# Kernel tuning notes

Hardware: AMD Instinct MI355X
Metric: run time of the kernel (lower is better)

## Reference

```python
import jax, jax.numpy as jnp
import numpy as np


def setup_inputs() -> dict:
    key = jax.random.key(0)
    kx, ke = jax.random.split(key)
    B, D, H, W, K = 64, 64, 32, 32, 512
    x = jax.random.normal(kx, (B, D, H, W), dtype=jnp.float32)
    # matches nn.init.normal_(weight, mean=0.0, std=2*D**-0.5)
    emb = jax.random.normal(ke, (D, K), dtype=jnp.float32) * (2.0 * D ** -0.5)
    return {"x": x, "emb": emb}


def reference(x, emb):
    # x: (B, D, *spatial), emb: (D, K)
    B, D = x.shape[0], x.shape[1]
    spatial = x.shape[2:]
    xf = jnp.moveaxis(x, 1, -1).reshape(B, -1, D)  # (B, N, D)
    scores = -2.0 * jnp.einsum('bnd,dk->bnk', xf, emb) + jnp.sum(emb * emb, axis=0)  # (B, N, K)
    argmin = jnp.argmin(scores, axis=-1)  # (B, N) int
    quant = jnp.take(emb.T, argmin, axis=0)  # (B, N, D) gather from codebook
    result = jnp.moveaxis(quant.reshape(B, *spatial, D), -1, 1)  # (B, D, *spatial)
    return result, argmin.reshape(B, *spatial)
```

## Files before the change

### kernel.cpp

```cpp
#include <hip/hip_runtime.h>


constexpr int D    = 64;
constexpr int K    = 512;
constexpr int HW   = 1024;
constexpr int ROWS = 64;
constexpr int CK   = 128;
constexpr int NCH  = K / CK;

__global__ __launch_bounds__(256, 3) void vq_kernel(
    const float* __restrict__ x,
    const float* __restrict__ emb,
    float* __restrict__ out_q,
    float* __restrict__ out_idx)
{
    __shared__ float xs[D][ROWS];
    __shared__ float es[D][CK];
    __shared__ float e2s[K];
    __shared__ int   kfin[ROWS];

    const int tid = threadIdx.x;
    const int ct  = tid & 15;
    const int rg  = tid >> 4;
    const int r0  = blockIdx.x * ROWS;
    const int b   = r0 >> 10;
    const int n0  = r0 & (HW - 1);

    const float* xg = x + ((size_t)b * D) * HW + n0;

    #pragma unroll
    for (int h = 0; h < 2; ++h) {
        const int k = h * 256 + tid;
        float s = 0.f;
        #pragma unroll
        for (int d = 0; d < D; ++d) {
            const float v = emb[d * K + k];
            s = fmaf(v, v, s);
        }
        e2s[k] = s;
    }

    #pragma unroll
    for (int p = 0; p < 4; ++p) {
        const int li = p * 256 + tid;
        const int d  = li >> 4;
        const int r4 = (li & 15) << 2;
        const float4 v = *reinterpret_cast<const float4*>(xg + (size_t)d * HW + r4);
        *reinterpret_cast<float4*>(&xs[d][r4]) = v;
    }

    float best[4] = {3.4e38f, 3.4e38f, 3.4e38f, 3.4e38f};
    int   bidx[4] = {0, 0, 0, 0};

    for (int ch = 0; ch < NCH; ++ch) {
        __syncthreads();

        #pragma unroll
        for (int p = 0; p < 8; ++p) {
            const int li = p * 256 + tid;
            const int d  = li >> 5;
            const int c4 = (li & 31) << 2;
            const float4 v = *reinterpret_cast<const float4*>(emb + d * K + ch * CK + c4);
            *reinterpret_cast<float4*>(&es[d][c4]) = v;
        }
        __syncthreads();

        float acc[4][8];
        #pragma unroll
        for (int j = 0; j < 4; ++j)
            #pragma unroll
            for (int i = 0; i < 8; ++i) acc[j][i] = 0.f;

        #pragma unroll
        for (int d = 0; d < D; ++d) {
            const float4 xv  = *reinterpret_cast<const float4*>(&xs[d][rg << 2]);
            const float4 ev0 = *reinterpret_cast<const float4*>(&es[d][ct << 3]);
            const float4 ev1 = *reinterpret_cast<const float4*>(&es[d][(ct << 3) + 4]);
            const float* xf  = reinterpret_cast<const float*>(&xv);
            const float* ef0 = reinterpret_cast<const float*>(&ev0);
            const float* ef1 = reinterpret_cast<const float*>(&ev1);
            #pragma unroll
            for (int j = 0; j < 4; ++j) {
                const float xj = xf[j];
                #pragma unroll
                for (int i = 0; i < 4; ++i) {
                    acc[j][i]     = fmaf(xj, ef0[i], acc[j][i]);
                    acc[j][i + 4] = fmaf(xj, ef1[i], acc[j][i + 4]);
                }
            }
        }

        const int kb = ch * CK + (ct << 3);
        const float4 q0 = *reinterpret_cast<const float4*>(&e2s[kb]);
        const float4 q1 = *reinterpret_cast<const float4*>(&e2s[kb + 4]);
        const float* qf0 = reinterpret_cast<const float*>(&q0);
        const float* qf1 = reinterpret_cast<const float*>(&q1);
        #pragma unroll
        for (int j = 0; j < 4; ++j) {
            #pragma unroll
            for (int i = 0; i < 8; ++i) {
                const float e2 = (i < 4) ? qf0[i] : qf1[i - 4];
                const float s  = fmaf(-2.f, acc[j][i], e2);
                if (s < best[j]) { best[j] = s; bidx[j] = kb + i; }
            }
        }
    }

    #pragma unroll
    for (int m = 1; m < 16; m <<= 1) {
        #pragma unroll
        for (int j = 0; j < 4; ++j) {
            const float ob = __shfl_xor(best[j], m, 64);
            const int   oi = __shfl_xor(bidx[j], m, 64);
            if (ob < best[j] || (ob == best[j] && oi < bidx[j])) {
                best[j] = ob; bidx[j] = oi;
            }
        }
    }

    if (ct == 0) {
        #pragma unroll
        for (int j = 0; j < 4; ++j) {
            kfin[(rg << 2) + j] = bidx[j];
            __builtin_nontemporal_store((float)bidx[j], &out_idx[r0 + (rg << 2) + j]);
        }
    }
    __syncthreads();

    const int row = tid & 63;
    const int dg  = tid >> 6;
    const int kq  = kfin[row];
    float* oq = out_q + ((size_t)b * D) * HW + n0 + row;
    #pragma unroll
    for (int j = 0; j < 16; ++j) {
        const int d = (dg << 4) + j;
        __builtin_nontemporal_store(emb[d * K + kq], &oq[(size_t)d * HW]);
    }
}

extern "C" void kernel_launch(void* const* d_in, const int* in_sizes, int n_in,
                              void* d_out, int out_size, void* d_ws, size_t ws_size,
                              hipStream_t stream)
{
    const float* x   = (const float*)d_in[0];
    const float* emb = (const float*)d_in[1];

    float* out_q   = (float*)d_out;
    float* out_idx = out_q + (size_t)64 * 64 * 1024;

    vq_kernel<<<1024, 256, 0, stream>>>(x, emb, out_q, out_idx);
}
```

Before: 127.7 us.

## Double rows per block to 8x8 register tiles and load LDS via global_load_lds

Each block now handles 128 rows instead of 64, so every thread holds an 8x8 accumulator tile over two strided row/code groups. This doubles reuse of each codebook chunk loaded into LDS and halves the grid to 512 blocks. The x and codebook tiles are loaded straight into LDS with global_load_lds instead of passing through registers. In exchange, register pressure rises (launch bounds drop to 2 blocks per CU) and fewer blocks are available for latency hiding.

```diff
diff --git a/kernel.cpp b/kernel.cpp
--- a/kernel.cpp
+++ b/kernel.cpp
@@ -4,11 +4,18 @@
 constexpr int D    = 64;
 constexpr int K    = 512;
 constexpr int HW   = 1024;
-constexpr int ROWS = 64;
+constexpr int ROWS = 128;
 constexpr int CK   = 128;
 constexpr int NCH  = K / CK;
 
-__global__ __launch_bounds__(256, 3) void vq_kernel(
+__device__ __forceinline__ void gload16(const float* g, float* l) {
+    __builtin_amdgcn_global_load_lds(
+        (const __attribute__((address_space(1))) void*)g,
+        (__attribute__((address_space(3))) void*)l,
+        16, 0, 0);
+}
+
+__global__ __launch_bounds__(256, 2) void vq_kernel(
     const float* __restrict__ x,
     const float* __restrict__ emb,
     float* __restrict__ out_q,
@@ -29,6 +36,14 @@
     const float* xg = x + ((size_t)b * D) * HW + n0;
 
     #pragma unroll
+    for (int p = 0; p < 8; ++p) {
+        const int li = p * 256 + tid;
+        const int d  = li >> 5;
+        const int r4 = (li & 31) << 2;
+        gload16(xg + (size_t)d * HW + r4, &xs[d][r4]);
+    }
+
+    #pragma unroll
     for (int h = 0; h < 2; ++h) {
         const int k = h * 256 + tid;
         float s = 0.f;
@@ -40,18 +55,12 @@
         e2s[k] = s;
     }
 
+    float best[8];
+    int   bidx[8];
     #pragma unroll
-    for (int p = 0; p < 4; ++p) {
-        const int li = p * 256 + tid;
-        const int d  = li >> 4;
-        const int r4 = (li & 15) << 2;
-        const float4 v = *reinterpret_cast<const float4*>(xg + (size_t)d * HW + r4);
-        *reinterpret_cast<float4*>(&xs[d][r4]) = v;
-    }
+    for (int j = 0; j < 8; ++j) { best[j] = 3.4e38f; bidx[j] = 0; }
 
-    float best[4] = {3.4e38f, 3.4e38f, 3.4e38f, 3.4e38f};
-    int   bidx[4] = {0, 0, 0, 0};
-
+    #pragma unroll 1
     for (int ch = 0; ch < NCH; ++ch) {
         __syncthreads();
 
@@ -60,48 +69,56 @@
             const int li = p * 256 + tid;
             const int d  = li >> 5;
             const int c4 = (li & 31) << 2;
-            const float4 v = *reinterpret_cast<const float4*>(emb + d * K + ch * CK + c4);
-            *reinterpret_cast<float4*>(&es[d][c4]) = v;
+            gload16(emb + d * K + ch * CK + c4, &es[d][c4]);
         }
         __syncthreads();
 
-        float acc[4][8];
+        float acc[8][8];
         #pragma unroll
-        for (int j = 0; j < 4; ++j)
+        for (int j = 0; j < 8; ++j)
             #pragma unroll
             for (int i = 0; i < 8; ++i) acc[j][i] = 0.f;
 
         #pragma unroll
         for (int d = 0; d < D; ++d) {
-            const float4 xv  = *reinterpret_cast<const float4*>(&xs[d][rg << 2]);
-            const float4 ev0 = *reinterpret_cast<const float4*>(&es[d][ct << 3]);
-            const float4 ev1 = *reinterpret_cast<const float4*>(&es[d][(ct << 3) + 4]);
-            const float* xf  = reinterpret_cast<const float*>(&xv);
-            const float* ef0 = reinterpret_cast<const float*>(&ev0);
-            const float* ef1 = reinterpret_cast<const float*>(&ev1);
+            const float4 xv0 = *reinterpret_cast<const float4*>(&xs[d][rg << 2]);
+            const float4 xv1 = *reinterpret_cast<const float4*>(&xs[d][64 + (rg << 2)]);
+            const float4 ev0 = *reinterpret_cast<const float4*>(&es[d][ct << 2]);
+            const float4 ev1 = *reinterpret_cast<const float4*>(&es[d][64 + (ct << 2)]);
+            const float* xa = reinterpret_cast<const float*>(&xv0);
+            const float* xb = reinterpret_cast<const float*>(&xv1);
+            const float* ea = reinterpret_cast<const float*>(&ev0);
+            const float* eb = reinterpret_cast<const float*>(&ev1);
             #pragma unroll
             for (int j = 0; j < 4; ++j) {
-                const float xj = xf[j];
+                const float x0 = xa[j];
+                const float x1 = xb[j];
                 #pragma unroll
                 for (int i = 0; i < 4; ++i) {
-                    acc[j][i]     = fmaf(xj, ef0[i], acc[j][i]);
-                    acc[j][i + 4] = fmaf(xj, ef1[i], acc[j][i + 4]);
+                    acc[j][i]         = fmaf(x0, ea[i], acc[j][i]);
+                    acc[j][i + 4]     = fmaf(x0, eb[i], acc[j][i + 4]);
+                    acc[j + 4][i]     = fmaf(x1, ea[i], acc[j + 4][i]);
+                    acc[j + 4][i + 4] = fmaf(x1, eb[i], acc[j + 4][i + 4]);
                 }
             }
         }
 
-        const int kb = ch * CK + (ct << 3);
-        const float4 q0 = *reinterpret_cast<const float4*>(&e2s[kb]);
-        const float4 q1 = *reinterpret_cast<const float4*>(&e2s[kb + 4]);
-        const float* qf0 = reinterpret_cast<const float*>(&q0);
-        const float* qf1 = reinterpret_cast<const float*>(&q1);
+        const int kb = ch * CK;
+        const float4 q0 = *reinterpret_cast<const float4*>(&e2s[kb + (ct << 2)]);
+        const float4 q1 = *reinterpret_cast<const float4*>(&e2s[kb + 64 + (ct << 2)]);
+        const float* qa = reinterpret_cast<const float*>(&q0);
+        const float* qb = reinterpret_cast<const float*>(&q1);
         #pragma unroll
-        for (int j = 0; j < 4; ++j) {
+        for (int j = 0; j < 8; ++j) {
             #pragma unroll
-            for (int i = 0; i < 8; ++i) {
-                const float e2 = (i < 4) ? qf0[i] : qf1[i - 4];
-                const float s  = fmaf(-2.f, acc[j][i], e2);
-                if (s < best[j]) { best[j] = s; bidx[j] = kb + i; }
+            for (int i = 0; i < 4; ++i) {
+                const float s0 = fmaf(-2.f, acc[j][i], qa[i]);
+                if (s0 < best[j]) { best[j] = s0; bidx[j] = kb + (ct << 2) + i; }
+            }
+            #pragma unroll
+            for (int i = 0; i < 4; ++i) {
+                const float s1 = fmaf(-2.f, acc[j][i + 4], qb[i]);
+                if (s1 < best[j]) { best[j] = s1; bidx[j] = kb + 64 + (ct << 2) + i; }
             }
         }
     }
@@ -109,7 +126,7 @@
     #pragma unroll
     for (int m = 1; m < 16; m <<= 1) {
         #pragma unroll
-        for (int j = 0; j < 4; ++j) {
+        for (int j = 0; j < 8; ++j) {
             const float ob = __shfl_xor(best[j], m, 64);
             const int   oi = __shfl_xor(bidx[j], m, 64);
             if (ob < best[j] || (ob == best[j] && oi < bidx[j])) {
@@ -120,20 +137,21 @@
 
     if (ct == 0) {
         #pragma unroll
-        for (int j = 0; j < 4; ++j) {
-            kfin[(rg << 2) + j] = bidx[j];
-            __builtin_nontemporal_store((float)bidx[j], &out_idx[r0 + (rg << 2) + j]);
+        for (int j = 0; j < 8; ++j) {
+            const int rloc = (j < 4) ? ((rg << 2) + j) : (64 + (rg << 2) + (j - 4));
+            kfin[rloc] = bidx[j];
+            __builtin_nontemporal_store((float)bidx[j], &out_idx[r0 + rloc]);
         }
     }
     __syncthreads();
 
-    const int row = tid & 63;
-    const int dg  = tid >> 6;
+    const int row = tid & 127;
+    const int dg  = tid >> 7;
     const int kq  = kfin[row];
     float* oq = out_q + ((size_t)b * D) * HW + n0 + row;
     #pragma unroll
-    for (int j = 0; j < 16; ++j) {
-        const int d = (dg << 4) + j;
+    for (int j = 0; j < 32; ++j) {
+        const int d = (dg << 5) + j;
         __builtin_nontemporal_store(emb[d * K + kq], &oq[(size_t)d * HW]);
     }
 }
@@ -148,5 +166,5 @@
     float* out_q   = (float*)d_out;
     float* out_idx = out_q + (size_t)64 * 64 * 1024;
 
-    vq_kernel<<<1024, 256, 0, stream>>>(x, emb, out_q, out_idx);
+    vq_kernel<<<512, 256, 0, stream>>>(x, emb, out_q, out_idx);
 }
```

Result: faster. 121.3 us (-5.0%).

## Drop LDS staging; read x and codebook directly with register prefetch

Applied to the files above, without the earlier changes.

Removes the shared-memory tiles for x and codebook chunks and the barriers around them. Each thread now loads its float4 slices of x and emb straight from global memory, prefetching the next codebook row in registers. The per-code squared norm is computed on the fly inside the dot-product loop. The register tile grows to 8x8 per thread with 256-wide chunks, and the index output store is coalesced through LDS. The risk is redundant global/L2 traffic, because many threads reread the same x and emb values, and higher register pressure against the new occupancy hint of 4.

```diff
diff --git a/kernel.cpp b/kernel.cpp
--- a/kernel.cpp
+++ b/kernel.cpp
@@ -5,127 +5,126 @@
 constexpr int K    = 512;
 constexpr int HW   = 1024;
 constexpr int ROWS = 64;
-constexpr int CK   = 128;
+constexpr int CK   = 256;
 constexpr int NCH  = K / CK;
 
-__global__ __launch_bounds__(256, 3) void vq_kernel(
+__global__ __launch_bounds__(256, 4) void vq_kernel(
     const float* __restrict__ x,
     const float* __restrict__ emb,
     float* __restrict__ out_q,
     float* __restrict__ out_idx)
 {
-    __shared__ float xs[D][ROWS];
-    __shared__ float es[D][CK];
-    __shared__ float e2s[K];
-    __shared__ int   kfin[ROWS];
+    __shared__ int kfin[ROWS];
 
     const int tid = threadIdx.x;
-    const int ct  = tid & 15;
-    const int rg  = tid >> 4;
+    const int ct  = tid & 31;
+    const int rg  = tid >> 5;
     const int r0  = blockIdx.x * ROWS;
     const int b   = r0 >> 10;
     const int n0  = r0 & (HW - 1);
 
-    const float* xg = x + ((size_t)b * D) * HW + n0;
+    const float* xp = x + ((size_t)b * D) * HW + n0 + (rg << 2);
 
+    float best[8];
+    int   bidx[8];
     #pragma unroll
-    for (int h = 0; h < 2; ++h) {
-        const int k = h * 256 + tid;
-        float s = 0.f;
+    for (int r = 0; r < 8; ++r) { best[r] = 3.4e38f; bidx[r] = 0; }
+
+    #pragma unroll 1
+    for (int ch = 0; ch < NCH; ++ch) {
+        const float* ep = emb + ch * CK + (ct << 2);
+
+        float acc[8][8];
         #pragma unroll
-        for (int d = 0; d < D; ++d) {
-            const float v = emb[d * K + k];
-            s = fmaf(v, v, s);
-        }
-        e2s[k] = s;
-    }
+        for (int r = 0; r < 8; ++r)
+            #pragma unroll
+            for (int c = 0; c < 8; ++c) acc[r][c] = 0.f;
+        float e2a[8];
+        #pragma unroll
+        for (int c = 0; c < 8; ++c) e2a[c] = 0.f;
 
-    #pragma unroll
-    for (int p = 0; p < 4; ++p) {
-        const int li = p * 256 + tid;
-        const int d  = li >> 4;
-        const int r4 = (li & 15) << 2;
-        const float4 v = *reinterpret_cast<const float4*>(xg + (size_t)d * HW + r4);
-        *reinterpret_cast<float4*>(&xs[d][r4]) = v;
-    }
-
-    float best[4] = {3.4e38f, 3.4e38f, 3.4e38f, 3.4e38f};
-    int   bidx[4] = {0, 0, 0, 0};
-
-    for (int ch = 0; ch < NCH; ++ch) {
-        __syncthreads();
-
-        #pragma unroll
-        for (int p = 0; p < 8; ++p) {
-            const int li = p * 256 + tid;
-            const int d  = li >> 5;
-            const int c4 = (li & 31) << 2;
-            const float4 v = *reinterpret_cast<const float4*>(emb + d * K + ch * CK + c4);
-            *reinterpret_cast<float4*>(&es[d][c4]) = v;
-        }
-        __syncthreads();
-
-        float acc[4][8];
-        #pragma unroll
-        for (int j = 0; j < 4; ++j)
+        auto step = [&](const float4& xa, const float4& xb,
+                        const float4& ea, const float4& eb) {
+            const float* xaf = reinterpret_cast<const float*>(&xa);
+            const float* xbf = reinterpret_cast<const float*>(&xb);
+            const float* eaf = reinterpret_cast<const float*>(&ea);
+            const float* ebf = reinterpret_cast<const float*>(&eb);
             #pragma unroll
-            for (int i = 0; i < 8; ++i) acc[j][i] = 0.f;
-
-        #pragma unroll
-        for (int d = 0; d < D; ++d) {
-            const float4 xv  = *reinterpret_cast<const float4*>(&xs[d][rg << 2]);
-            const float4 ev0 = *reinterpret_cast<const float4*>(&es[d][ct << 3]);
-            const float4 ev1 = *reinterpret_cast<const float4*>(&es[d][(ct << 3) + 4]);
-            const float* xf  = reinterpret_cast<const float*>(&xv);
-            const float* ef0 = reinterpret_cast<const float*>(&ev0);
-            const float* ef1 = reinterpret_cast<const float*>(&ev1);
+            for (int c = 0; c < 4; ++c) {
+                e2a[c]     = fmaf(eaf[c], eaf[c], e2a[c]);
+                e2a[4 + c] = fmaf(ebf[c], ebf[c], e2a[4 + c]);
+            }
             #pragma unroll
-            for (int j = 0; j < 4; ++j) {
-                const float xj = xf[j];
+            for (int r = 0; r < 4; ++r) {
+                const float x0 = xaf[r];
+                const float x1 = xbf[r];
                 #pragma unroll
-                for (int i = 0; i < 4; ++i) {
-                    acc[j][i]     = fmaf(xj, ef0[i], acc[j][i]);
-                    acc[j][i + 4] = fmaf(xj, ef1[i], acc[j][i + 4]);
+                for (int c = 0; c < 4; ++c) {
+                    acc[r][c]         = fmaf(x0, eaf[c], acc[r][c]);
+                    acc[r][4 + c]     = fmaf(x0, ebf[c], acc[r][4 + c]);
+                    acc[r + 4][c]     = fmaf(x1, eaf[c], acc[r + 4][c]);
+                    acc[r + 4][4 + c] = fmaf(x1, ebf[c], acc[r + 4][4 + c]);
                 }
             }
+        };
+
+        float4 ea = *reinterpret_cast<const float4*>(ep);
+        float4 eb = *reinterpret_cast<const float4*>(ep + 128);
+
+        #pragma unroll 9
+        for (int d = 0; d < D - 1; ++d) {
+            const float4 xa  = *reinterpret_cast<const float4*>(xp + (size_t)d * HW);
+            const float4 xb  = *reinterpret_cast<const float4*>(xp + (size_t)d * HW + 32);
+            const float4 nea = *reinterpret_cast<const float4*>(ep + (d + 1) * K);
+            const float4 neb = *reinterpret_cast<const float4*>(ep + (d + 1) * K + 128);
+            step(xa, xb, ea, eb);
+            ea = nea; eb = neb;
+        }
+        {
+            const float4 xa = *reinterpret_cast<const float4*>(xp + (size_t)(D - 1) * HW);
+            const float4 xb = *reinterpret_cast<const float4*>(xp + (size_t)(D - 1) * HW + 32);
+            step(xa, xb, ea, eb);
         }
 
-        const int kb = ch * CK + (ct << 3);
-        const float4 q0 = *reinterpret_cast<const float4*>(&e2s[kb]);
-        const float4 q1 = *reinterpret_cast<const float4*>(&e2s[kb + 4]);
-        const float* qf0 = reinterpret_cast<const float*>(&q0);
-        const float* qf1 = reinterpret_cast<const float*>(&q1);
+        const int kb = ch * CK + (ct << 2);
         #pragma unroll
-        for (int j = 0; j < 4; ++j) {
+        for (int r = 0; r < 8; ++r) {
             #pragma unroll
-            for (int i = 0; i < 8; ++i) {
-                const float e2 = (i < 4) ? qf0[i] : qf1[i - 4];
-                const float s  = fmaf(-2.f, acc[j][i], e2);
-                if (s < best[j]) { best[j] = s; bidx[j] = kb + i; }
+            for (int c = 0; c < 4; ++c) {
+                const float s = fmaf(-2.f, acc[r][c], e2a[c]);
+                if (s < best[r]) { best[r] = s; bidx[r] = kb + c; }
+            }
+            #pragma unroll
+            for (int c = 0; c < 4; ++c) {
+                const float s = fmaf(-2.f, acc[r][4 + c], e2a[4 + c]);
+                if (s < best[r]) { best[r] = s; bidx[r] = kb + 128 + c; }
             }
         }
     }
 
     #pragma unroll
-    for (int m = 1; m < 16; m <<= 1) {
+    for (int m = 1; m < 32; m <<= 1) {
         #pragma unroll
-        for (int j = 0; j < 4; ++j) {
-            const float ob = __shfl_xor(best[j], m, 64);
-            const int   oi = __shfl_xor(bidx[j], m, 64);
-            if (ob < best[j] || (ob == best[j] && oi < bidx[j])) {
-                best[j] = ob; bidx[j] = oi;
+        for (int r = 0; r < 8; ++r) {
+            const float ob = __shfl_xor(best[r], m, 64);
+            const int   oi = __shfl_xor(bidx[r], m, 64);
+            if (ob < best[r] || (ob == best[r] && oi < bidx[r])) {
+                best[r] = ob; bidx[r] = oi;
             }
         }
     }
 
     if (ct == 0) {
         #pragma unroll
-        for (int j = 0; j < 4; ++j) {
-            kfin[(rg << 2) + j] = bidx[j];
-            __builtin_nontemporal_store((float)bidx[j], &out_idx[r0 + (rg << 2) + j]);
+        for (int r = 0; r < 4; ++r) {
+            kfin[(rg << 2) + r]      = bidx[r];
+            kfin[32 + (rg << 2) + r] = bidx[4 + r];
         }
     }
     __syncthreads();
+
+    if (tid < ROWS)
+        __builtin_nontemporal_store((float)kfin[tid], &out_idx[r0 + tid]);
 
     const int row = tid & 63;
     const int dg  = tid >> 6;
```

Result: slower. 243.3 us (+90.6%).
